# Kernel optimization log

Measured on AMD Instinct MI355X. Metric: run time of the kernel, lower is better.

## Reference

```python
import jax, jax.numpy as jnp
import numpy as np

N, E = 100000, 1600000
D_IN, D_H, D_OUT = 32, 64, 1


def _init_linear(key, fan_in, fan_out):
    k1, k2 = jax.random.split(key)
    lim = 1.0 / np.sqrt(fan_in)
    w = jax.random.uniform(k1, (fan_in, fan_out), minval=-lim, maxval=lim, dtype=jnp.float32)
    b = jax.random.uniform(k2, (fan_out,), minval=-lim, maxval=lim, dtype=jnp.float32)
    return w, b


def setup_inputs() -> dict:
    key = jax.random.key(0)
    ks = jax.random.split(key, 8)
    x = jax.random.normal(ks[0], (N, D_IN), dtype=jnp.float32)
    edge_index = jax.random.randint(ks[1], (2, E), 0, N, dtype=jnp.int64)
    w1_rel, b1 = _init_linear(ks[2], D_IN, D_H)
    w1_root, _ = _init_linear(ks[3], D_IN, D_H)
    w2_rel, b2 = _init_linear(ks[4], D_H, D_H)
    w2_root, _ = _init_linear(ks[5], D_H, D_H)
    w3_rel, b3 = _init_linear(ks[6], D_H, D_OUT)
    w3_root, _ = _init_linear(ks[7], D_H, D_OUT)
    return {
        "x": x,
        "w1_rel": w1_rel, "b1": b1, "w1_root": w1_root,
        "w2_rel": w2_rel, "b2": b2, "w2_root": w2_root,
        "w3_rel": w3_rel, "b3": b3, "w3_root": w3_root,
        "edge_index": edge_index,
    }


def _graph_conv(x, edge_index, w_rel, b_rel, w_root):
    # PyG GraphConv: out_i = W_rel @ (sum_{j->i} x_j) + b_rel + W_root @ x_i
    src, dst = edge_index[0], edge_index[1]
    agg = jax.ops.segment_sum(x[src], dst, num_segments=x.shape[0])  # [N, d]
    return agg @ w_rel + b_rel + x @ w_root


def reference(x, w1_rel, b1, w1_root, w2_rel, b2, w2_root, w3_rel, b3, w3_root, edge_index):
    # Dropout is inactive in eval mode (F.dropout with training=False is identity).
    h = jax.nn.relu(_graph_conv(x, edge_index, w1_rel, b1, w1_root))
    h = jax.nn.relu(_graph_conv(h, edge_index, w2_rel, b2, w2_root))
    out = _graph_conv(h, edge_index, w3_rel, b3, w3_root)
    return out.reshape(-1)  # [N], since output_dim == 1
```

## Files before the change

kernel.cpp:

```cpp
#include <hip/hip_runtime.h>
#include <hip/hip_fp16.h>

typedef _Float16 f16x8 __attribute__((ext_vector_type(8)));
typedef float    f32x4 __attribute__((ext_vector_type(4)));

constexpr int DIN = 32;
constexpr int DH  = 64;
constexpr int NBSHIFT = 8;
constexpr int TILE_A  = 4096;
constexpr int FB_CAP  = 6144;


__global__ __launch_bounds__(256) void k_setup(
    const float2* __restrict__ x2, __half2* __restrict__ xh,
    const float* __restrict__ w1_rel, const float* __restrict__ w1_root,
    const float* __restrict__ w2_rel, const float* __restrict__ w2_root,
    __half* __restrict__ wf1, __half* __restrict__ wf2,
    int* __restrict__ ch, int n2) {
  int i = blockIdx.x * 256 + threadIdx.x;
  if (i < n2) {
    float2 v = x2[i];
    xh[i] = __floats2half2_rn(v.x, v.y);
    return;
  }
  int u = i - n2;
  if (u < 512) {
    int lane = u & 63, kt = (u >> 6) & 1, mt = u >> 7;
    int out = 16 * mt + (lane & 15);
    int kb = 32 * kt + (lane >> 4) * 8;
    union { uint4 q; __half h[8]; } pk;
#pragma unroll
    for (int j = 0; j < 8; ++j) {
      int k = kb + j;
      float w = (k < 32) ? w1_root[k * DH + out] : w1_rel[(k - 32) * DH + out];
      pk.h[j] = __float2half(w);
    }
    *(uint4*)(wf1 + (size_t)u * 8) = pk.q;
    return;
  }
  u -= 512;
  if (u < 1024) {
    int lane = u & 63, kt = (u >> 6) & 3, mt = u >> 8;
    int out = 16 * mt + (lane & 15);
    int kb = 32 * kt + (lane >> 4) * 8;
    union { uint4 q; __half h[8]; } pk;
#pragma unroll
    for (int j = 0; j < 8; ++j) {
      int k = kb + j;
      float w = (k < 64) ? w2_rel[k * DH + out] : w2_root[(k - 64) * DH + out];
      pk.h[j] = __float2half(w);
    }
    *(uint4*)(wf2 + (size_t)u * 8) = pk.q;
    return;
  }
  u -= 1024;
  if (u < 512) ch[u] = 0;
}


__global__ __launch_bounds__(256) void k_chist(
    const int* __restrict__ dst, int* __restrict__ ch, int E, int nbuckets) {
  __shared__ int hist[512];
  long long t0 = (long long)blockIdx.x * TILE_A;
  int cnt = (int)min((long long)TILE_A, (long long)E - t0);
  for (int i = threadIdx.x; i < nbuckets; i += 256) hist[i] = 0;
  __syncthreads();
  for (int r = threadIdx.x; r < cnt; r += 256)
    atomicAdd(&hist[dst[t0 + r] >> NBSHIFT], 1);
  __syncthreads();
  for (int i = threadIdx.x; i < nbuckets; i += 256)
    if (hist[i]) atomicAdd(&ch[i], hist[i]);
}

__global__ __launch_bounds__(256) void k_cscan(
    const int* __restrict__ ch, int* __restrict__ cb, int* __restrict__ bcur,
    int nbuckets, int E) {
  __shared__ int ts[256];
  int i0 = threadIdx.x * 2, i1 = i0 + 1;
  int v0 = (i0 < nbuckets) ? ch[i0] : 0;
  int v1 = (i1 < nbuckets) ? ch[i1] : 0;
  int s = v0 + v1;
  ts[threadIdx.x] = s;
  __syncthreads();
  for (int off = 1; off < 256; off <<= 1) {
    int val = (threadIdx.x >= off) ? ts[threadIdx.x - off] : 0;
    __syncthreads();
    ts[threadIdx.x] += val;
    __syncthreads();
  }
  int ex = ts[threadIdx.x] - s;
  if (i0 < nbuckets) { cb[i0] = ex;      bcur[i0] = ex; }
  if (i1 < nbuckets) { cb[i1] = ex + v0; bcur[i1] = ex + v0; }
  if (threadIdx.x == 255) cb[nbuckets] = E;
}

__global__ __launch_bounds__(256) void k_binA(
    const int* __restrict__ src, const int* __restrict__ dst,
    int* __restrict__ bcur, unsigned* __restrict__ bin,
    int E, int nbuckets) {
  __shared__ int hist[512];
  __shared__ int lbase[512];
  __shared__ int gbase[512];
  __shared__ int ts[256];
  __shared__ unsigned lsort[TILE_A];
  __shared__ unsigned short lbuck[TILE_A];
  long long t0 = (long long)blockIdx.x * TILE_A;
  int cnt = (int)min((long long)TILE_A, (long long)E - t0);
  for (int i = threadIdx.x; i < 512; i += 256) hist[i] = 0;
  __syncthreads();
  unsigned pk[TILE_A / 256];
  int bo[TILE_A / 256];
#pragma unroll
  for (int q = 0; q < TILE_A / 256; ++q) {
    int r = (int)threadIdx.x + q * 256;
    if (r < cnt) {
      int d = dst[t0 + r];
      int s = src[t0 + r];
      int b = d >> NBSHIFT;
      int off = atomicAdd(&hist[b], 1);
      pk[q] = ((unsigned)(d & 255) << 17) | (unsigned)s;
      bo[q] = (b << 16) | off;
    }
  }
  __syncthreads();
  {
    int i0 = threadIdx.x * 2, i1 = i0 + 1;
    int v0 = hist[i0], v1 = hist[i1];
    int s2 = v0 + v1;
    ts[threadIdx.x] = s2;
    __syncthreads();
    for (int off = 1; off < 256; off <<= 1) {
      int val = (threadIdx.x >= off) ? ts[threadIdx.x - off] : 0;
      __syncthreads();
      ts[threadIdx.x] += val;
      __syncthreads();
    }
    int ex = ts[threadIdx.x] - s2;
    lbase[i0] = ex;
    lbase[i1] = ex + v0;
    gbase[i0] = v0 ? atomicAdd(&bcur[i0], v0) : 0;
    gbase[i1] = v1 ? atomicAdd(&bcur[i1], v1) : 0;
  }
  __syncthreads();
#pragma unroll
  for (int q = 0; q < TILE_A / 256; ++q) {
    int r = (int)threadIdx.x + q * 256;
    if (r < cnt) {
      int b = bo[q] >> 16, off = bo[q] & 0xFFFF;
      int li = lbase[b] + off;
      lsort[li] = pk[q];
      lbuck[li] = (unsigned short)b;
    }
  }
  __syncthreads();
  for (int i = threadIdx.x; i < cnt; i += 256) {
    int b = lbuck[i];
    bin[gbase[b] + (i - lbase[b])] = lsort[i];
  }
}

__global__ __launch_bounds__(256) void k_fillB(
    const unsigned* __restrict__ bin, const int* __restrict__ cb,
    int* __restrict__ rp, int* __restrict__ ssrc, int n, int E) {
  __shared__ int deg[256];
  __shared__ int ts[256];
  __shared__ int cur[256];
  __shared__ int lsort[FB_CAP];
  int b = blockIdx.x;
  int nbase = b << NBSHIFT;
  int nn = min(256, n - nbase);
  int ebeg = cb[b], eend = cb[b + 1];
  int cnt = eend - ebeg;
  deg[threadIdx.x] = 0;
  __syncthreads();
  for (int e = ebeg + (int)threadIdx.x; e < eend; e += 256)
    atomicAdd(&deg[bin[e] >> 17], 1);
  __syncthreads();
  int d = deg[threadIdx.x];
  ts[threadIdx.x] = d;
  __syncthreads();
  for (int off = 1; off < 256; off <<= 1) {
    int val = (threadIdx.x >= off) ? ts[threadIdx.x - off] : 0;
    __syncthreads();
    ts[threadIdx.x] += val;
    __syncthreads();
  }
  int pref = ts[threadIdx.x] - d;
  if ((int)threadIdx.x < nn) rp[nbase + threadIdx.x] = ebeg + pref;
  if (b == 0 && threadIdx.x == 0) rp[n] = E;
  cur[threadIdx.x] = pref;
  __syncthreads();
  if (cnt <= FB_CAP) {
    for (int e = ebeg + (int)threadIdx.x; e < eend; e += 256) {
      unsigned u = bin[e];
      int pos = atomicAdd(&cur[u >> 17], 1);
      lsort[pos] = (int)(u & 0x1FFFF);
    }
    __syncthreads();
    for (int i = threadIdx.x; i < cnt; i += 256)
      ssrc[ebeg + i] = lsort[i];
  } else {
    for (int e = ebeg + (int)threadIdx.x; e < eend; e += 256) {
      unsigned u = bin[e];
      int pos = atomicAdd(&cur[u >> 17], 1);
      ssrc[ebeg + pos] = (int)(u & 0x1FFFF);
    }
  }
}

__global__ __launch_bounds__(256) void k_l1fused(
    const _Float16* __restrict__ X, const int* __restrict__ rp,
    const int* __restrict__ ssrc, const _Float16* __restrict__ WF,
    const float* __restrict__ b1, _Float16* __restrict__ H1, int n) {
  __shared__ _Float16 sagg[64][40];
  int tid = threadIdx.x;
  int nl = tid >> 2;
  int unit = tid & 3;
  int nodeg = blockIdx.x * 64 + nl;
  {
    f16x8 accA = (f16x8)(_Float16)0.0f;
    f16x8 accB = (f16x8)(_Float16)0.0f;
    if (nodeg < n) {
      int beg = rp[nodeg], end = rp[nodeg + 1];
      const f16x8* fx = (const f16x8*)X;
      int e = beg;
      for (; e + 7 < end; e += 8) {
        int s0 = ssrc[e],     s1 = ssrc[e + 1], s2 = ssrc[e + 2], s3 = ssrc[e + 3];
        int s4 = ssrc[e + 4], s5 = ssrc[e + 5], s6 = ssrc[e + 6], s7 = ssrc[e + 7];
        f16x8 v0 = fx[(size_t)s0 * 4 + unit];
        f16x8 v1 = fx[(size_t)s1 * 4 + unit];
        f16x8 v2 = fx[(size_t)s2 * 4 + unit];
        f16x8 v3 = fx[(size_t)s3 * 4 + unit];
        f16x8 v4 = fx[(size_t)s4 * 4 + unit];
        f16x8 v5 = fx[(size_t)s5 * 4 + unit];
        f16x8 v6 = fx[(size_t)s6 * 4 + unit];
        f16x8 v7 = fx[(size_t)s7 * 4 + unit];
        accA += v0; accB += v1; accA += v2; accB += v3;
        accA += v4; accB += v5; accA += v6; accB += v7;
      }
      for (; e + 1 < end; e += 2) {
        int s0 = ssrc[e], s1 = ssrc[e + 1];
        f16x8 v0 = fx[(size_t)s0 * 4 + unit];
        f16x8 v1 = fx[(size_t)s1 * 4 + unit];
        accA += v0; accB += v1;
      }
      if (e < end) accA += fx[(size_t)ssrc[e] * 4 + unit];
    }
    *(f16x8*)&sagg[nl][unit * 8] = accA + accB;
  }
  __syncthreads();
  int lane = tid & 63;
  int w = tid >> 6;
  int nl16 = w * 16 + (lane & 15);
  int node = blockIdx.x * 64 + nl16;
  int nodeld = min(node, n - 1);
  f16x8 bf0 = *(const f16x8*)(X + (size_t)nodeld * 32 + (lane >> 4) * 8);
  f16x8 bf1 = *(const f16x8*)&sagg[nl16][(lane >> 4) * 8];
  const f16x8* ap = (const f16x8*)WF + lane;
  f32x4 acc[4];
#pragma unroll
  for (int mt = 0; mt < 4; ++mt) acc[mt] = (f32x4)(0.f);
#pragma unroll
  for (int mt = 0; mt < 4; ++mt) {
    acc[mt] = __builtin_amdgcn_mfma_f32_16x16x32_f16(ap[(mt * 2 + 0) * 64], bf0, acc[mt], 0, 0, 0);
    acc[mt] = __builtin_amdgcn_mfma_f32_16x16x32_f16(ap[(mt * 2 + 1) * 64], bf1, acc[mt], 0, 0, 0);
  }
  if (node >= n) return;
  int jb = (lane >> 4) * 4;
  _Float16* op = H1 + (size_t)node * 64 + jb;
#pragma unroll
  for (int mt = 0; mt < 4; ++mt) {
    f32x4 vb = *(const f32x4*)(b1 + 16 * mt + jb);
    union { uint2 u2; _Float16 h[4]; } pko;
#pragma unroll
    for (int r = 0; r < 4; ++r)
      pko.h[r] = (_Float16)fmaxf(acc[mt][r] + vb[r], 0.f);
    *(uint2*)(op + 16 * mt) = pko.u2;
  }
}

__global__ __launch_bounds__(256) void k_l2fused(
    const _Float16* __restrict__ H1, const int* __restrict__ rp,
    const int* __restrict__ ssrc, const _Float16* __restrict__ WF,
    const float* __restrict__ b2, const float* __restrict__ w3rel,
    const float* __restrict__ w3root,
    float* __restrict__ S, float* __restrict__ T, int n) {
  __shared__ _Float16 sagg[64][72];
  int tid = threadIdx.x;
  int nl = tid >> 2;
  int u0 = tid & 3;
  int nodeg = blockIdx.x * 64 + nl;
  {
    f16x8 aA = (f16x8)(_Float16)0.0f, aB = (f16x8)(_Float16)0.0f;
    f16x8 cA = (f16x8)(_Float16)0.0f, cB = (f16x8)(_Float16)0.0f;
    if (nodeg < n) {
      int beg = rp[nodeg], end = rp[nodeg + 1];
      const f16x8* fh = (const f16x8*)H1;
      int e = beg;
      for (; e + 7 < end; e += 8) {
        int s0 = ssrc[e],     s1 = ssrc[e + 1], s2 = ssrc[e + 2], s3 = ssrc[e + 3];
        int s4 = ssrc[e + 4], s5 = ssrc[e + 5], s6 = ssrc[e + 6], s7 = ssrc[e + 7];
        f16x8 a0 = fh[(size_t)s0 * 8 + u0];
        f16x8 c0 = fh[(size_t)s0 * 8 + u0 + 4];
        f16x8 a1 = fh[(size_t)s1 * 8 + u0];
        f16x8 c1 = fh[(size_t)s1 * 8 + u0 + 4];
        f16x8 a2 = fh[(size_t)s2 * 8 + u0];
        f16x8 c2 = fh[(size_t)s2 * 8 + u0 + 4];
        f16x8 a3 = fh[(size_t)s3 * 8 + u0];
        f16x8 c3 = fh[(size_t)s3 * 8 + u0 + 4];
        f16x8 a4 = fh[(size_t)s4 * 8 + u0];
        f16x8 c4 = fh[(size_t)s4 * 8 + u0 + 4];
        f16x8 a5 = fh[(size_t)s5 * 8 + u0];
        f16x8 c5 = fh[(size_t)s5 * 8 + u0 + 4];
        f16x8 a6 = fh[(size_t)s6 * 8 + u0];
        f16x8 c6 = fh[(size_t)s6 * 8 + u0 + 4];
        f16x8 a7 = fh[(size_t)s7 * 8 + u0];
        f16x8 c7 = fh[(size_t)s7 * 8 + u0 + 4];
        aA += a0; cA += c0; aB += a1; cB += c1;
        aA += a2; cA += c2; aB += a3; cB += c3;
        aA += a4; cA += c4; aB += a5; cB += c5;
        aA += a6; cA += c6; aB += a7; cB += c7;
      }
      for (; e + 1 < end; e += 2) {
        int s0 = ssrc[e], s1 = ssrc[e + 1];
        aA += fh[(size_t)s0 * 8 + u0];
        cA += fh[(size_t)s0 * 8 + u0 + 4];
        aB += fh[(size_t)s1 * 8 + u0];
        cB += fh[(size_t)s1 * 8 + u0 + 4];
      }
      if (e < end) {
        int s0 = ssrc[e];
        aA += fh[(size_t)s0 * 8 + u0];
        cA += fh[(size_t)s0 * 8 + u0 + 4];
      }
    }
    *(f16x8*)&sagg[nl][u0 * 8] = aA + aB;
    *(f16x8*)&sagg[nl][(u0 + 4) * 8] = cA + cB;
  }
  __syncthreads();
  int lane = tid & 63;
  int w = tid >> 6;
  int nl16 = w * 16 + (lane & 15);
  int node = blockIdx.x * 64 + nl16;
  int nodeld = min(node, n - 1);
  f16x8 bf[4];
  bf[0] = *(const f16x8*)&sagg[nl16][(lane >> 4) * 8];
  bf[1] = *(const f16x8*)&sagg[nl16][32 + (lane >> 4) * 8];
  bf[2] = *(const f16x8*)(H1 + (size_t)nodeld * 64 + (lane >> 4) * 8);
  bf[3] = *(const f16x8*)(H1 + (size_t)nodeld * 64 + 32 + (lane >> 4) * 8);
  const f16x8* ap = (const f16x8*)WF + lane;
  f32x4 acc[4];
#pragma unroll
  for (int mt = 0; mt < 4; ++mt) acc[mt] = (f32x4)(0.f);
#pragma unroll
  for (int mt = 0; mt < 4; ++mt)
#pragma unroll
    for (int kt = 0; kt < 4; ++kt)
      acc[mt] = __builtin_amdgcn_mfma_f32_16x16x32_f16(
          ap[(mt * 4 + kt) * 64], bf[kt], acc[mt], 0, 0, 0);
  int jb = (lane >> 4) * 4;
  float s = 0.f, t = 0.f;
#pragma unroll
  for (int mt = 0; mt < 4; ++mt) {
    f32x4 vb = *(const f32x4*)(b2 + 16 * mt + jb);
    f32x4 vr = *(const f32x4*)(w3rel + 16 * mt + jb);
    f32x4 vt = *(const f32x4*)(w3root + 16 * mt + jb);
#pragma unroll
    for (int r = 0; r < 4; ++r) {
      float h = fmaxf(acc[mt][r] + vb[r], 0.f);
      s = fmaf(h, vr[r], s);
      t = fmaf(h, vt[r], t);
    }
  }
  s += __shfl_xor(s, 16); s += __shfl_xor(s, 32);
  t += __shfl_xor(t, 16); t += __shfl_xor(t, 32);
  if (lane < 16 && node < n) { S[node] = s; T[node] = t; }
}


__global__ __launch_bounds__(256) void k_final(
    const float* __restrict__ sv, const int* __restrict__ rp,
    const int* __restrict__ ssrc, const float* __restrict__ T,
    const float* __restrict__ b3, float* __restrict__ out, int n) {
  int t = blockIdx.x * 256 + threadIdx.x;
  int node = t >> 2;
  int l = t & 3;
  if (node >= n) return;
  int beg = rp[node], end = rp[node + 1];
  float a = 0.f;
  for (int e = beg + l; e < end; e += 4) a += sv[ssrc[e]];
  a += __shfl_xor(a, 1);
  a += __shfl_xor(a, 2);
  if (l == 0) out[node] = a + b3[0] + T[node];
}


extern "C" void kernel_launch(void* const* d_in, const int* in_sizes, int n_in,
                              void* d_out, int out_size, void* d_ws, size_t ws_size,
                              hipStream_t stream) {
  const float* x       = (const float*)d_in[0];
  const float* w1_rel  = (const float*)d_in[1];
  const float* b1      = (const float*)d_in[2];
  const float* w1_root = (const float*)d_in[3];
  const float* w2_rel  = (const float*)d_in[4];
  const float* b2      = (const float*)d_in[5];
  const float* w2_root = (const float*)d_in[6];
  const float* w3_rel  = (const float*)d_in[7];
  const float* b3      = (const float*)d_in[8];
  const float* w3_root = (const float*)d_in[9];
  const int*   edge    = (const int*)d_in[10];

  const int n = in_sizes[0] / DIN;
  const int E = in_sizes[10] / 2;
  const int* src = edge;
  const int* dst = edge + E;

  _Float16* XH = (_Float16*)d_ws;
  _Float16* H1 = XH + (size_t)n * 32;
  float*    S  = (float*)(H1 + (size_t)n * 64);
  float*    T  = S + n;
  int* RP   = (int*)(T + n);
  int* SSRC = RP + ((n + 8) & ~7);
  int* CH   = SSRC + E;
  int* CB   = CH + 512;
  int* BCUR = CB + 520;
  __half* WF1 = (__half*)(BCUR + 512);
  __half* WF2 = WF1 + 4096;
  unsigned* BIN = (unsigned*)H1;

  const int B = 256;
  const int nbuckets = (n + 255) >> NBSHIFT;
  const int gA = (E + TILE_A - 1) / TILE_A;
  const int gF = (n + 63) / 64;

  {
    int n2 = n * 16;
    int tot = n2 + 2048;
    k_setup<<<(tot + B - 1) / B, B, 0, stream>>>(
        (const float2*)x, (__half2*)XH, w1_rel, w1_root, w2_rel, w2_root,
        WF1, WF2, CH, n2);
  }

  k_chist<<<gA, B, 0, stream>>>(dst, CH, E, nbuckets);
  k_cscan<<<1, B, 0, stream>>>(CH, CB, BCUR, nbuckets, E);
  k_binA<<<gA, B, 0, stream>>>(src, dst, BCUR, BIN, E, nbuckets);
  k_fillB<<<nbuckets, B, 0, stream>>>(BIN, CB, RP, SSRC, n, E);

  k_l1fused<<<gF, B, 0, stream>>>(XH, RP, SSRC, (const _Float16*)WF1, b1, H1, n);
  k_l2fused<<<gF, B, 0, stream>>>(H1, RP, SSRC, (const _Float16*)WF2,
                                  b2, w3_rel, w3_root, S, T, n);

  k_final<<<(4 * n + B - 1) / B, B, 0, stream>>>(S, RP, SSRC, T, b3, (float*)d_out, n);
}
```

Baseline: 135.9 us.

## Fuse histogram into setup and layer-1 aggregation into CSR fill kernel

Merges the x conversion, weight packing and dst-bucket histogram into one prep kernel that writes per-tile histograms, so no zeroing or global atomics are needed; the scan now sums these tiles. Layer-1 aggregation and MFMA run inside the CSR fill kernel, reading neighbour indices straight from shared memory instead of re-reading rp/ssrc from global memory. BIN moves to its own workspace region because H1 is now written while BIN is still in use. In exchange, the fused kernel runs only one block per 256 nodes (about 391 blocks), which lowers parallelism for the gather, and the scan serially loops over roughly 390 tile rows.

```diff
diff --git a/kernel.cpp b/kernel.cpp
--- a/kernel.cpp
+++ b/kernel.cpp
@@ -10,88 +10,88 @@
 constexpr int TILE_A  = 4096;
 constexpr int FB_CAP  = 6144;
 
-
-__global__ __launch_bounds__(256) void k_setup(
-    const float2* __restrict__ x2, __half2* __restrict__ xh,
+__global__ __launch_bounds__(256) void k_prep(
+    const int* __restrict__ dst, const float2* __restrict__ x2,
+    __half2* __restrict__ xh,
     const float* __restrict__ w1_rel, const float* __restrict__ w1_root,
     const float* __restrict__ w2_rel, const float* __restrict__ w2_root,
     __half* __restrict__ wf1, __half* __restrict__ wf2,
-    int* __restrict__ ch, int n2) {
-  int i = blockIdx.x * 256 + threadIdx.x;
-  if (i < n2) {
+    int* __restrict__ cht, int E, int n2) {
+  __shared__ int hist[512];
+  int tid = threadIdx.x, b = blockIdx.x;
+  long long t0 = (long long)b * TILE_A;
+  int cnt = (int)min((long long)TILE_A, (long long)E - t0);
+  if (cnt < 0) cnt = 0;
+  for (int i = tid; i < 512; i += 256) hist[i] = 0;
+  __syncthreads();
+  for (int r = tid; r < cnt; r += 256)
+    atomicAdd(&hist[dst[t0 + r] >> NBSHIFT], 1);
+  __syncthreads();
+  for (int i = tid; i < 512; i += 256) cht[b * 512 + i] = hist[i];
+  for (int i = b * 256 + tid; i < n2; i += gridDim.x * 256) {
     float2 v = x2[i];
     xh[i] = __floats2half2_rn(v.x, v.y);
-    return;
-  }
-  int u = i - n2;
-  if (u < 512) {
-    int lane = u & 63, kt = (u >> 6) & 1, mt = u >> 7;
-    int out = 16 * mt + (lane & 15);
-    int kb = 32 * kt + (lane >> 4) * 8;
-    union { uint4 q; __half h[8]; } pk;
-#pragma unroll
-    for (int j = 0; j < 8; ++j) {
-      int k = kb + j;
-      float w = (k < 32) ? w1_root[k * DH + out] : w1_rel[(k - 32) * DH + out];
-      pk.h[j] = __float2half(w);
-    }
-    *(uint4*)(wf1 + (size_t)u * 8) = pk.q;
-    return;
-  }
-  u -= 512;
-  if (u < 1024) {
-    int lane = u & 63, kt = (u >> 6) & 3, mt = u >> 8;
-    int out = 16 * mt + (lane & 15);
-    int kb = 32 * kt + (lane >> 4) * 8;
-    union { uint4 q; __half h[8]; } pk;
-#pragma unroll
-    for (int j = 0; j < 8; ++j) {
-      int k = kb + j;
-      float w = (k < 64) ? w2_rel[k * DH + out] : w2_root[(k - 64) * DH + out];
-      pk.h[j] = __float2half(w);
-    }
-    *(uint4*)(wf2 + (size_t)u * 8) = pk.q;
-    return;
-  }
-  u -= 1024;
-  if (u < 512) ch[u] = 0;
-}
-
-
-__global__ __launch_bounds__(256) void k_chist(
-    const int* __restrict__ dst, int* __restrict__ ch, int E, int nbuckets) {
-  __shared__ int hist[512];
-  long long t0 = (long long)blockIdx.x * TILE_A;
-  int cnt = (int)min((long long)TILE_A, (long long)E - t0);
-  for (int i = threadIdx.x; i < nbuckets; i += 256) hist[i] = 0;
-  __syncthreads();
-  for (int r = threadIdx.x; r < cnt; r += 256)
-    atomicAdd(&hist[dst[t0 + r] >> NBSHIFT], 1);
-  __syncthreads();
-  for (int i = threadIdx.x; i < nbuckets; i += 256)
-    if (hist[i]) atomicAdd(&ch[i], hist[i]);
+  }
+  if (b == 1) {
+    for (int u = tid; u < 512; u += 256) {
+      int lane = u & 63, kt = (u >> 6) & 1, mt = u >> 7;
+      int outc = 16 * mt + (lane & 15);
+      int kb = 32 * kt + (lane >> 4) * 8;
+      union { uint4 q; __half h[8]; } w;
+#pragma unroll
+      for (int j = 0; j < 8; ++j) {
+        int k = kb + j;
+        float wv = (k < 32) ? w1_root[k * DH + outc] : w1_rel[(k - 32) * DH + outc];
+        w.h[j] = __float2half(wv);
+      }
+      *(uint4*)(wf1 + (size_t)u * 8) = w.q;
+    }
+  } else if (b == 2) {
+    for (int u = tid; u < 1024; u += 256) {
+      int lane = u & 63, kt = (u >> 6) & 3, mt = u >> 8;
+      int outc = 16 * mt + (lane & 15);
+      int kb = 32 * kt + (lane >> 4) * 8;
+      union { uint4 q; __half h[8]; } w;
+#pragma unroll
+      for (int j = 0; j < 8; ++j) {
+        int k = kb + j;
+        float wv = (k < 64) ? w2_rel[k * DH + outc] : w2_root[(k - 64) * DH + outc];
+        w.h[j] = __float2half(wv);
+      }
+      *(uint4*)(wf2 + (size_t)u * 8) = w.q;
+    }
+  }
 }
 
 __global__ __launch_bounds__(256) void k_cscan(
-    const int* __restrict__ ch, int* __restrict__ cb, int* __restrict__ bcur,
-    int nbuckets, int E) {
+    const int* __restrict__ cht, int* __restrict__ cb, int* __restrict__ bcur,
+    int ntiles) {
+  __shared__ int sbk[512];
   __shared__ int ts[256];
-  int i0 = threadIdx.x * 2, i1 = i0 + 1;
-  int v0 = (i0 < nbuckets) ? ch[i0] : 0;
-  int v1 = (i1 < nbuckets) ? ch[i1] : 0;
-  int s = v0 + v1;
-  ts[threadIdx.x] = s;
+  int tid = threadIdx.x;
+  int s0 = 0, s1 = 0;
+  for (int t = 0; t < ntiles; ++t) {
+    const int* row = cht + (size_t)t * 512;
+    s0 += row[tid];
+    s1 += row[tid + 256];
+  }
+  sbk[tid] = s0;
+  sbk[tid + 256] = s1;
+  __syncthreads();
+  int i0 = tid * 2, i1 = i0 + 1;
+  int v0 = sbk[i0], v1 = sbk[i1];
+  int s2 = v0 + v1;
+  ts[tid] = s2;
   __syncthreads();
   for (int off = 1; off < 256; off <<= 1) {
-    int val = (threadIdx.x >= off) ? ts[threadIdx.x - off] : 0;
-    __syncthreads();
-    ts[threadIdx.x] += val;
-    __syncthreads();
-  }
-  int ex = ts[threadIdx.x] - s;
-  if (i0 < nbuckets) { cb[i0] = ex;      bcur[i0] = ex; }
-  if (i1 < nbuckets) { cb[i1] = ex + v0; bcur[i1] = ex + v0; }
-  if (threadIdx.x == 255) cb[nbuckets] = E;
+    int val = (tid >= off) ? ts[tid - off] : 0;
+    __syncthreads();
+    ts[tid] += val;
+    __syncthreads();
+  }
+  int ex = ts[tid] - s2;
+  cb[i0] = ex;      bcur[i0] = ex;
+  cb[i1] = ex + v0; bcur[i1] = ex + v0;
 }
 
 __global__ __launch_bounds__(256) void k_binA(
@@ -159,123 +159,137 @@
   }
 }
 
-__global__ __launch_bounds__(256) void k_fillB(
+__global__ __launch_bounds__(256) void k_fillB_l1(
     const unsigned* __restrict__ bin, const int* __restrict__ cb,
-    int* __restrict__ rp, int* __restrict__ ssrc, int n, int E) {
+    int* __restrict__ rp, int* __restrict__ ssrc,
+    const _Float16* __restrict__ X, const _Float16* __restrict__ WF1,
+    const float* __restrict__ b1, _Float16* __restrict__ H1, int n, int E) {
   __shared__ int deg[256];
   __shared__ int ts[256];
   __shared__ int cur[256];
-  __shared__ int lsort[FB_CAP];
+  __shared__ int ubuf[FB_CAP];
+  __shared__ _Float16 sagg[64 * 40];
   int b = blockIdx.x;
+  int tid = threadIdx.x;
   int nbase = b << NBSHIFT;
   int nn = min(256, n - nbase);
   int ebeg = cb[b], eend = cb[b + 1];
   int cnt = eend - ebeg;
-  deg[threadIdx.x] = 0;
-  __syncthreads();
-  for (int e = ebeg + (int)threadIdx.x; e < eend; e += 256)
+  deg[tid] = 0;
+  __syncthreads();
+  for (int e = ebeg + tid; e < eend; e += 256)
     atomicAdd(&deg[bin[e] >> 17], 1);
   __syncthreads();
-  int d = deg[threadIdx.x];
-  ts[threadIdx.x] = d;
+  int d = deg[tid];
+  ts[tid] = d;
   __syncthreads();
   for (int off = 1; off < 256; off <<= 1) {
-    int val = (threadIdx.x >= off) ? ts[threadIdx.x - off] : 0;
-    __syncthreads();
-    ts[threadIdx.x] += val;
-    __syncthreads();
-  }
-  int pref = ts[threadIdx.x] - d;
-  if ((int)threadIdx.x < nn) rp[nbase + threadIdx.x] = ebeg + pref;
-  if (b == 0 && threadIdx.x == 0) rp[n] = E;
-  cur[threadIdx.x] = pref;
-  __syncthreads();
-  if (cnt <= FB_CAP) {
-    for (int e = ebeg + (int)threadIdx.x; e < eend; e += 256) {
+    int val = (tid >= off) ? ts[tid - off] : 0;
+    __syncthreads();
+    ts[tid] += val;
+    __syncthreads();
+  }
+  int pref = ts[tid] - d;
+  if (tid < nn) rp[nbase + tid] = ebeg + pref;
+  if (b == 0 && tid == 0) rp[n] = E;
+  cur[tid] = pref;
+  __syncthreads();
+  bool fit = (cnt <= FB_CAP);
+  if (fit) {
+    for (int e = ebeg + tid; e < eend; e += 256) {
       unsigned u = bin[e];
       int pos = atomicAdd(&cur[u >> 17], 1);
-      lsort[pos] = (int)(u & 0x1FFFF);
-    }
-    __syncthreads();
-    for (int i = threadIdx.x; i < cnt; i += 256)
-      ssrc[ebeg + i] = lsort[i];
+      ubuf[pos] = (int)(u & 0x1FFFF);
+    }
+    __syncthreads();
+    for (int i = tid; i < cnt; i += 256)
+      ssrc[ebeg + i] = ubuf[i];
   } else {
-    for (int e = ebeg + (int)threadIdx.x; e < eend; e += 256) {
+    for (int e = ebeg + tid; e < eend; e += 256) {
       unsigned u = bin[e];
       int pos = atomicAdd(&cur[u >> 17], 1);
       ssrc[ebeg + pos] = (int)(u & 0x1FFFF);
     }
-  }
-}
-
-__global__ __launch_bounds__(256) void k_l1fused(
-    const _Float16* __restrict__ X, const int* __restrict__ rp,
-    const int* __restrict__ ssrc, const _Float16* __restrict__ WF,
-    const float* __restrict__ b1, _Float16* __restrict__ H1, int n) {
-  __shared__ _Float16 sagg[64][40];
-  int tid = threadIdx.x;
-  int nl = tid >> 2;
-  int unit = tid & 3;
-  int nodeg = blockIdx.x * 64 + nl;
-  {
-    f16x8 accA = (f16x8)(_Float16)0.0f;
-    f16x8 accB = (f16x8)(_Float16)0.0f;
-    if (nodeg < n) {
-      int beg = rp[nodeg], end = rp[nodeg + 1];
-      const f16x8* fx = (const f16x8*)X;
-      int e = beg;
-      for (; e + 7 < end; e += 8) {
-        int s0 = ssrc[e],     s1 = ssrc[e + 1], s2 = ssrc[e + 2], s3 = ssrc[e + 3];
-        int s4 = ssrc[e + 4], s5 = ssrc[e + 5], s6 = ssrc[e + 6], s7 = ssrc[e + 7];
-        f16x8 v0 = fx[(size_t)s0 * 4 + unit];
-        f16x8 v1 = fx[(size_t)s1 * 4 + unit];
-        f16x8 v2 = fx[(size_t)s2 * 4 + unit];
-        f16x8 v3 = fx[(size_t)s3 * 4 + unit];
-        f16x8 v4 = fx[(size_t)s4 * 4 + unit];
-        f16x8 v5 = fx[(size_t)s5 * 4 + unit];
-        f16x8 v6 = fx[(size_t)s6 * 4 + unit];
-        f16x8 v7 = fx[(size_t)s7 * 4 + unit];
-        accA += v0; accB += v1; accA += v2; accB += v3;
-        accA += v4; accB += v5; accA += v6; accB += v7;
-      }
-      for (; e + 1 < end; e += 2) {
-        int s0 = ssrc[e], s1 = ssrc[e + 1];
-        f16x8 v0 = fx[(size_t)s0 * 4 + unit];
-        f16x8 v1 = fx[(size_t)s1 * 4 + unit];
-        accA += v0; accB += v1;
-      }
-      if (e < end) accA += fx[(size_t)ssrc[e] * 4 + unit];
-    }
-    *(f16x8*)&sagg[nl][unit * 8] = accA + accB;
-  }
-  __syncthreads();
+    __syncthreads();
+  }
+  __syncthreads();
+
+  const f16x8* fx = (const f16x8*)X;
   int lane = tid & 63;
   int w = tid >> 6;
-  int nl16 = w * 16 + (lane & 15);
-  int node = blockIdx.x * 64 + nl16;
-  int nodeld = min(node, n - 1);
-  f16x8 bf0 = *(const f16x8*)(X + (size_t)nodeld * 32 + (lane >> 4) * 8);
-  f16x8 bf1 = *(const f16x8*)&sagg[nl16][(lane >> 4) * 8];
-  const f16x8* ap = (const f16x8*)WF + lane;
-  f32x4 acc[4];
-#pragma unroll
-  for (int mt = 0; mt < 4; ++mt) acc[mt] = (f32x4)(0.f);
-#pragma unroll
-  for (int mt = 0; mt < 4; ++mt) {
-    acc[mt] = __builtin_amdgcn_mfma_f32_16x16x32_f16(ap[(mt * 2 + 0) * 64], bf0, acc[mt], 0, 0, 0);
-    acc[mt] = __builtin_amdgcn_mfma_f32_16x16x32_f16(ap[(mt * 2 + 1) * 64], bf1, acc[mt], 0, 0, 0);
-  }
-  if (node >= n) return;
-  int jb = (lane >> 4) * 4;
-  _Float16* op = H1 + (size_t)node * 64 + jb;
-#pragma unroll
-  for (int mt = 0; mt < 4; ++mt) {
-    f32x4 vb = *(const f32x4*)(b1 + 16 * mt + jb);
-    union { uint2 u2; _Float16 h[4]; } pko;
-#pragma unroll
-    for (int r = 0; r < 4; ++r)
-      pko.h[r] = (_Float16)fmaxf(acc[mt][r] + vb[r], 0.f);
-    *(uint2*)(op + 16 * mt) = pko.u2;
+  for (int sub = 0; sub < 4; ++sub) {
+    int nl = tid >> 2;
+    int unit = tid & 3;
+    int ln = sub * 64 + nl;
+    {
+      f16x8 accA = (f16x8)(_Float16)0.0f;
+      f16x8 accB = (f16x8)(_Float16)0.0f;
+      if (ln < nn) {
+        int beg = ts[ln] - deg[ln];
+        int end = ts[ln];
+        int e = beg;
+        if (fit) {
+          for (; e + 7 < end; e += 8) {
+            int s0 = ubuf[e],     s1 = ubuf[e + 1], s2 = ubuf[e + 2], s3 = ubuf[e + 3];
+            int s4 = ubuf[e + 4], s5 = ubuf[e + 5], s6 = ubuf[e + 6], s7 = ubuf[e + 7];
+            f16x8 v0 = fx[(size_t)s0 * 4 + unit];
+            f16x8 v1 = fx[(size_t)s1 * 4 + unit];
+            f16x8 v2 = fx[(size_t)s2 * 4 + unit];
+            f16x8 v3 = fx[(size_t)s3 * 4 + unit];
+            f16x8 v4 = fx[(size_t)s4 * 4 + unit];
+            f16x8 v5 = fx[(size_t)s5 * 4 + unit];
+            f16x8 v6 = fx[(size_t)s6 * 4 + unit];
+            f16x8 v7 = fx[(size_t)s7 * 4 + unit];
+            accA += v0; accB += v1; accA += v2; accB += v3;
+            accA += v4; accB += v5; accA += v6; accB += v7;
+          }
+          for (; e + 1 < end; e += 2) {
+            f16x8 v0 = fx[(size_t)ubuf[e] * 4 + unit];
+            f16x8 v1 = fx[(size_t)ubuf[e + 1] * 4 + unit];
+            accA += v0; accB += v1;
+          }
+          if (e < end) accA += fx[(size_t)ubuf[e] * 4 + unit];
+        } else {
+          const int* gs = ssrc + ebeg;
+          for (; e + 1 < end; e += 2) {
+            f16x8 v0 = fx[(size_t)gs[e] * 4 + unit];
+            f16x8 v1 = fx[(size_t)gs[e + 1] * 4 + unit];
+            accA += v0; accB += v1;
+          }
+          if (e < end) accA += fx[(size_t)gs[e] * 4 + unit];
+        }
+      }
+      *(f16x8*)&sagg[nl * 40 + unit * 8] = accA + accB;
+    }
+    __syncthreads();
+    int nl16 = w * 16 + (lane & 15);
+    int node = nbase + sub * 64 + nl16;
+    int nodeld = min(node, n - 1);
+    f16x8 bf0 = *(const f16x8*)(X + (size_t)nodeld * 32 + (lane >> 4) * 8);
+    f16x8 bf1 = *(const f16x8*)&sagg[nl16 * 40 + (lane >> 4) * 8];
+    const f16x8* ap = (const f16x8*)WF1 + lane;
+    f32x4 acc[4];
+#pragma unroll
+    for (int mt = 0; mt < 4; ++mt) acc[mt] = (f32x4)(0.f);
+#pragma unroll
+    for (int mt = 0; mt < 4; ++mt) {
+      acc[mt] = __builtin_amdgcn_mfma_f32_16x16x32_f16(ap[(mt * 2 + 0) * 64], bf0, acc[mt], 0, 0, 0);
+      acc[mt] = __builtin_amdgcn_mfma_f32_16x16x32_f16(ap[(mt * 2 + 1) * 64], bf1, acc[mt], 0, 0, 0);
+    }
+    if (node < n) {
+      int jb = (lane >> 4) * 4;
+      _Float16* op = H1 + (size_t)node * 64 + jb;
+#pragma unroll
+      for (int mt = 0; mt < 4; ++mt) {
+        f32x4 vb = *(const f32x4*)(b1 + 16 * mt + jb);
+        union { uint2 u2; _Float16 h[4]; } pko;
+#pragma unroll
+        for (int r = 0; r < 4; ++r)
+          pko.h[r] = (_Float16)fmaxf(acc[mt][r] + vb[r], 0.f);
+        *(uint2*)(op + 16 * mt) = pko.u2;
+      }
+    }
+    __syncthreads();
   }
 }
 
@@ -377,7 +391,6 @@
   if (lane < 16 && node < n) { S[node] = s; T[node] = t; }
 }
 
-
 __global__ __launch_bounds__(256) void k_final(
     const float* __restrict__ sv, const int* __restrict__ rp,
     const int* __restrict__ ssrc, const float* __restrict__ T,
@@ -421,34 +434,27 @@
   float*    T  = S + n;
   int* RP   = (int*)(T + n);
   int* SSRC = RP + ((n + 8) & ~7);
-  int* CH   = SSRC + E;
-  int* CB   = CH + 512;
+  unsigned* BIN = (unsigned*)(SSRC + E);
+  int* CB   = (int*)(BIN + E);
   int* BCUR = CB + 520;
   __half* WF1 = (__half*)(BCUR + 512);
   __half* WF2 = WF1 + 4096;
-  unsigned* BIN = (unsigned*)H1;
+  int* CHT = (int*)(WF2 + 8192);
 
   const int B = 256;
   const int nbuckets = (n + 255) >> NBSHIFT;
-  const int gA = (E + TILE_A - 1) / TILE_A;
+  const int ntiles = (E + TILE_A - 1) / TILE_A;
   const int gF = (n + 63) / 64;
-
-  {
-    int n2 = n * 16;
-    int tot = n2 + 2048;
-    k_setup<<<(tot + B - 1) / B, B, 0, stream>>>(
-        (const float2*)x, (__half2*)XH, w1_rel, w1_root, w2_rel, w2_root,
-        WF1, WF2, CH, n2);
-  }
-
-  k_chist<<<gA, B, 0, stream>>>(dst, CH, E, nbuckets);
-  k_cscan<<<1, B, 0, stream>>>(CH, CB, BCUR, nbuckets, E);
-  k_binA<<<gA, B, 0, stream>>>(src, dst, BCUR, BIN, E, nbuckets);
-  k_fillB<<<nbuckets, B, 0, stream>>>(BIN, CB, RP, SSRC, n, E);
-
-  k_l1fused<<<gF, B, 0, stream>>>(XH, RP, SSRC, (const _Float16*)WF1, b1, H1, n);
+  int n2 = n * 16;
+
+  k_prep<<<ntiles, B, 0, stream>>>(dst, (const float2*)x, (__half2*)XH,
+                                   w1_rel, w1_root, w2_rel, w2_root,
+                                   WF1, WF2, CHT, E, n2);
+  k_cscan<<<1, B, 0, stream>>>(CHT, CB, BCUR, ntiles);
+  k_binA<<<ntiles, B, 0, stream>>>(src, dst, BCUR, BIN, E, nbuckets);
+  k_fillB_l1<<<nbuckets, B, 0, stream>>>(BIN, CB, RP, SSRC,
+                                         XH, (const _Float16*)WF1, b1, H1, n, E);
   k_l2fused<<<gF, B, 0, stream>>>(H1, RP, SSRC, (const _Float16*)WF2,
                                   b2, w3_rel, w3_root, S, T, n);
-
   k_final<<<(4 * n + B - 1) / B, B, 0, stream>>>(S, RP, SSRC, T, b3, (float*)d_out, n);
 }
```

Measured after the change: 179.6 us. +32.2%, slower.
